# Performance work log

Hardware: AMD Instinct MI355X
Metric: run time of the kernel (lower is better)

The kernel has to match this reference:

```python
import jax, jax.numpy as jnp
import numpy as np

N = 100000      # nodes
E = 1600000     # edges (before self-loops)
IN = 256        # in_channels
HID = 16        # num_hid (per-head channels, layer 1)
HEADS = 4
OUT = 16        # out_channels (per-head channels, layer 2)
NEG_SLOPE = 0.2 # PyG GATConv default


def setup_inputs() -> dict:
    key = jax.random.key(0)
    ks = jax.random.split(key, 12)
    def glorot(k, shape, fan):
        return jax.random.normal(k, shape, jnp.float32) * (1.0 / np.sqrt(fan))
    x = jax.random.normal(ks[0], (N, IN), jnp.float32)
    edge_index = jax.random.randint(ks[1], (2, E), 0, N, dtype=jnp.int32)
    W1 = glorot(ks[2], (IN, HEADS * HID), IN)
    att_src1 = glorot(ks[3], (HEADS, HID), HID)
    att_dst1 = glorot(ks[4], (HEADS, HID), HID)
    b1 = jnp.zeros((HEADS * HID,), jnp.float32)
    W2 = glorot(ks[5], (HEADS * HID, HEADS * OUT), HEADS * HID)
    att_src2 = glorot(ks[6], (HEADS, OUT), OUT)
    att_dst2 = glorot(ks[7], (HEADS, OUT), OUT)
    b2 = jnp.zeros((HEADS * OUT,), jnp.float32)
    return {"x": x, "edge_index": edge_index, "W1": W1, "att_src1": att_src1,
            "att_dst1": att_dst1, "b1": b1, "W2": W2, "att_src2": att_src2,
            "att_dst2": att_dst2, "b2": b2}


def gat_conv(x, W, att_src, att_dst, bias, src, dst):
    # PyG GATConv (concat=True): h = xW per head; alpha via segment-softmax over dst.
    H, C = att_src.shape
    n = x.shape[0]
    h = (x @ W).reshape(n, H, C)                    # [N,H,C]
    a_s = jnp.sum(h * att_src, axis=-1)             # [N,H]
    a_d = jnp.sum(h * att_dst, axis=-1)             # [N,H]
    e = jax.nn.leaky_relu(a_s[src] + a_d[dst], NEG_SLOPE)  # [E',H]
    m = jax.lax.stop_gradient(jax.ops.segment_max(e, dst, num_segments=n))
    p = jnp.exp(e - m[dst])
    s = jax.ops.segment_sum(p, dst, num_segments=n)
    alpha = p / (s[dst] + 1e-16)                    # [E',H]
    msg = h[src] * alpha[:, :, None]                # [E',H,C] gathered messages
    out = jax.ops.segment_sum(msg, dst, num_segments=n)
    return out.reshape(n, H * C) + bias


def reference(x, edge_index, W1, att_src1, att_dst1, b1, W2, att_src2, att_dst2, b2):
    # add self loops (PyG GATConv default add_self_loops=True)
    loops = jnp.arange(N, dtype=edge_index.dtype)
    src = jnp.concatenate([edge_index[0], loops])
    dst = jnp.concatenate([edge_index[1], loops])
    h = jax.nn.relu(gat_conv(x, W1, att_src1, att_dst1, b1, src, dst))
    # dropout is identity in eval mode
    return gat_conv(h, W2, att_src2, att_dst2, b2, src, dst)
```

## Files before the change

### kernel.cpp

```cpp
#include <hip/hip_runtime.h>
#include <hip/hip_fp16.h>
#include <cstdint>


#define CH 4096
#define MAXB 512
#define SCAP 6144

using f16x8 = __attribute__((ext_vector_type(8))) _Float16;
using f32x4 = __attribute__((ext_vector_type(4))) float;

__device__ __forceinline__ float lrelu(float v) { return fmaxf(v, 0.2f * v); }

__global__ void ifill_kernel(int* __restrict__ p, int v, int n) {
  int i = blockIdx.x * blockDim.x + threadIdx.x;
  if (i < n) p[i] = v;
}

__global__ void wprep2_kernel(const float* __restrict__ W,
                              const float* __restrict__ as,
                              const float* __restrict__ ad,
                              ushort* __restrict__ WT, int K) {
  int i = blockIdx.x * 256 + threadIdx.x;
  if (i >= 80 * K) return;
  int c = i / K, k = i % K;
  float v = 0.f;
  if (c < 64) {
    v = W[k * 64 + c];
  } else if (c < 68) {
    int hd = c - 64;
    for (int j = 0; j < 16; ++j) v += W[k * 64 + hd * 16 + j] * as[hd * 16 + j];
  } else if (c < 72) {
    int hd = c - 68;
    for (int j = 0; j < 16; ++j) v += W[k * 64 + hd * 16 + j] * ad[hd * 16 + j];
  }
  WT[c * K + k] = __half_as_ushort(__float2half_rn(v));
}

__global__ __launch_bounds__(256) void bucket_hist(const int* __restrict__ edst,
                                                   int E, int nbuck,
                                                   int* __restrict__ bucket_cnt) {
  __shared__ int hist[MAXB];
  const int t = threadIdx.x;
  for (int j = t; j < MAXB; j += 256) hist[j] = 0;
  __syncthreads();
  const int base = blockIdx.x * CH;
#pragma unroll
  for (int k = 0; k < CH / 256; ++k) {
    int e = base + k * 256 + t;
    if (e < E) atomicAdd(&hist[edst[e] >> 8], 1);
  }
  __syncthreads();
  for (int j = t; j < nbuck; j += 256) {
    int c = hist[j];
    if (c) atomicAdd(&bucket_cnt[j], c);
  }
}

__global__ __launch_bounds__(512) void bucket_scan(const int* __restrict__ bucket_cnt,
                                                   int* __restrict__ bucket_base,
                                                   int* __restrict__ bucket_cursor,
                                                   int nbuck) {
  __shared__ int part[512];
  const int t = threadIdx.x;
  int v = (t < nbuck) ? bucket_cnt[t] : 0;
  part[t] = v;
  __syncthreads();
  for (int off = 1; off < 512; off <<= 1) {
    int u = (t >= off) ? part[t - off] : 0;
    __syncthreads();
    part[t] += u;
    __syncthreads();
  }
  int ex = part[t] - v;
  if (t <= nbuck) {
    int w = (t < nbuck) ? ex : part[nbuck - 1];
    bucket_base[t] = w;
    if (t < nbuck) bucket_cursor[t] = w;
  }
}

__global__ __launch_bounds__(256) void place_kernel(const int* __restrict__ esrc,
                                                    const int* __restrict__ edst,
                                                    int E, int nbuck,
                                                    int* __restrict__ bucket_cursor,
                                                    unsigned int* __restrict__ pairs) {
  __shared__ int hist[MAXB];
  __shared__ int gbase[MAXB];
  __shared__ int rcnt[MAXB];
  const int t = threadIdx.x;
  for (int j = t; j < MAXB; j += 256) { hist[j] = 0; rcnt[j] = 0; }
  __syncthreads();
  const int base = blockIdx.x * CH;
  int b_[CH / 256];
  unsigned int p_[CH / 256];
#pragma unroll
  for (int k = 0; k < CH / 256; ++k) {
    int e = base + k * 256 + t;
    if (e < E) {
      int d = edst[e];
      int s = esrc[e];
      b_[k] = d >> 8;
      p_[k] = ((unsigned int)s << 8) | (unsigned int)(d & 255);
      atomicAdd(&hist[b_[k]], 1);
    } else {
      b_[k] = -1;
    }
  }
  __syncthreads();
  for (int j = t; j < nbuck; j += 256) {
    int c = hist[j];
    gbase[j] = c ? atomicAdd(&bucket_cursor[j], c) : 0;
  }
  __syncthreads();
#pragma unroll
  for (int k = 0; k < CH / 256; ++k) {
    if (b_[k] >= 0) {
      int r = atomicAdd(&rcnt[b_[k]], 1);
      pairs[gbase[b_[k]] + r] = p_[k];
    }
  }
}

__global__ __launch_bounds__(256) void bucket_build(
    const unsigned int* __restrict__ pairs, const int* __restrict__ bucket_base,
    int* __restrict__ ccol, int* __restrict__ start, int* __restrict__ endp,
    int n) {
  __shared__ int cnt[256];
  __shared__ int ls[256];
  __shared__ int csave[256];
  __shared__ int part[256];
  __shared__ int sorted[SCAP];
  const int t = threadIdx.x;
  const int b = blockIdx.x;
  const int d0 = b << 8;
  const int DR = min(256, n - d0);
  const int in_base = bucket_base[b];
  const int nloc = bucket_base[b + 1] - in_base;
  const int out_base = in_base + d0;

  cnt[t] = (t < DR) ? 1 : 0;
  __syncthreads();
  for (int i = t; i < nloc; i += 256)
    atomicAdd(&cnt[pairs[in_base + i] & 255u], 1);
  __syncthreads();
  int c = cnt[t];
  csave[t] = c;
  part[t] = c;
  __syncthreads();
#pragma unroll
  for (int off = 1; off < 256; off <<= 1) {
    int u = (t >= off) ? part[t - off] : 0;
    __syncthreads();
    part[t] += u;
    __syncthreads();
  }
  ls[t] = part[t] - c;
  __syncthreads();
  if (t < DR) {
    int s = out_base + ls[t];
    start[d0 + t] = s;
    endp[d0 + t] = s + csave[t];
    sorted[ls[t]] = d0 + t;
    cnt[t] = 1;
  }
  __syncthreads();
  for (int i = t; i < nloc; i += 256) {
    unsigned int p = pairs[in_base + i];
    int j = (int)(p & 255u);
    int r = atomicAdd(&cnt[j], 1);
    int pos = ls[j] + r;
    if (pos < SCAP) sorted[pos] = (int)(p >> 8);
  }
  __syncthreads();
  int tot = nloc + DR;
  if (tot > SCAP) tot = SCAP;
  for (int i = t; i < tot; i += 256) ccol[out_base + i] = sorted[i];
}

__global__ __launch_bounds__(256) void gemm1_mfma(
    const float* __restrict__ x, const ushort* __restrict__ wt,
    __half* __restrict__ h, float* __restrict__ as_, float* __restrict__ ad_,
    int n) {
  constexpr int K = 256, NS = K / 32;
  __shared__ _Float16 hs[64 * 88];
  __shared__ float att[64 * 12];
  const int tid = threadIdx.x;
  const int w = tid >> 6;
  const int lane = tid & 63;
  const int lr = lane & 15;
  const int kg = lane >> 4;
  const int row0 = blockIdx.x * 64;

  int rr = row0 + w * 16 + lr;
  if (rr > n - 1) rr = n - 1;

  const ushort* wbase = wt + lr * K + kg * 8;

  f16x8 af[NS];
  {
    float4 av[NS][2];
    const float* xp = x + (long long)rr * K + kg * 8;
#pragma unroll
    for (int s = 0; s < NS; ++s) {
      av[s][0] = *(const float4*)(xp + s * 32);
      av[s][1] = *(const float4*)(xp + s * 32 + 4);
    }
#pragma unroll
    for (int s = 0; s < NS; ++s) {
      af[s][0] = (_Float16)av[s][0].x; af[s][1] = (_Float16)av[s][0].y;
      af[s][2] = (_Float16)av[s][0].z; af[s][3] = (_Float16)av[s][0].w;
      af[s][4] = (_Float16)av[s][1].x; af[s][5] = (_Float16)av[s][1].y;
      af[s][6] = (_Float16)av[s][1].z; af[s][7] = (_Float16)av[s][1].w;
    }
  }

  f32x4 acc[5] = {};
#pragma unroll
  for (int s = 0; s < NS; ++s)
#pragma unroll
    for (int ct = 0; ct < 5; ++ct) {
      f16x8 b = *(const f16x8*)(wbase + ct * 16 * K + s * 32);
      acc[ct] = __builtin_amdgcn_mfma_f32_16x16x32_f16(af[s], b, acc[ct], 0, 0, 0);
    }

  const int orow = w * 16 + kg * 4;
#pragma unroll
  for (int ct = 0; ct < 4; ++ct)
#pragma unroll
    for (int r = 0; r < 4; ++r)
      hs[(orow + r) * 88 + ct * 16 + lr] = (_Float16)acc[ct][r];
  if (lr < 8) {
#pragma unroll
    for (int r = 0; r < 4; ++r)
      att[(orow + r) * 12 + lr] = acc[4][r];
  }
  __syncthreads();
#pragma unroll
  for (int j = 0; j < 2; ++j) {
    int s = tid + j * 256;
    int row = s >> 3, seg = s & 7;
    if (row0 + row < n)
      *(uint4*)(h + (long long)(row0 + row) * 64 + seg * 8) =
          *(const uint4*)&hs[row * 88 + seg * 8];
  }
  if (tid < 64) {
    if (row0 + tid < n)
      *(float4*)(as_ + (long long)(row0 + tid) * 4) = *(const float4*)&att[tid * 12];
  } else if (tid < 128) {
    int t2 = tid - 64;
    if (row0 + t2 < n)
      *(float4*)(ad_ + (long long)(row0 + t2) * 4) = *(const float4*)&att[t2 * 12 + 4];
  }
}

__global__ __launch_bounds__(256) void agg1_kernel(
    const int* __restrict__ ccol, const int* __restrict__ start,
    const int* __restrict__ endp,
    const float* __restrict__ as1, const float* __restrict__ ad1,
    const __half2* __restrict__ h2in, const float* __restrict__ bias,
    const float* __restrict__ W2, const float* __restrict__ a2s,
    const float* __restrict__ a2d,
    __half2* __restrict__ h2out, float* __restrict__ as2,
    float* __restrict__ ad2, int n) {
  __shared__ float x2s[8][65];
  __shared__ __half2 w2s[64 * 32];
  const int t = threadIdx.x;
  for (int i = t; i < 2048; i += 256) {
    float2 wv = *(const float2*)(W2 + i * 2);
    w2s[i] = __floats2half2_rn(wv.x, wv.y);
  }

  const int lw = t >> 5;
  const int hl = t & 31;
  const int hh = hl >> 3;
  const int node = blockIdx.x * 8 + lw;
  const bool act = node < n;
  const int nodec = act ? node : 0;

  const float adv = ad1[nodec * 4 + hh];
  const int s0i = start[nodec];
  const int d = act ? (endp[nodec] - s0i) : 0;
  const int* cp = ccol + s0i;
  float ax = 0.f, ay = 0.f, den = 0.f;
  int i = 0;
  for (; i + 4 <= d; i += 4) {
    int s0 = cp[i], s1 = cp[i + 1], s2 = cp[i + 2], s3 = cp[i + 3];
    float p0 = __expf(lrelu(as1[s0 * 4 + hh] + adv));
    float p1 = __expf(lrelu(as1[s1 * 4 + hh] + adv));
    float p2 = __expf(lrelu(as1[s2 * 4 + hh] + adv));
    float p3 = __expf(lrelu(as1[s3 * 4 + hh] + adv));
    float2 h0 = __half22float2(h2in[s0 * 32 + hl]);
    float2 h1 = __half22float2(h2in[s1 * 32 + hl]);
    float2 h2v = __half22float2(h2in[s2 * 32 + hl]);
    float2 h3 = __half22float2(h2in[s3 * 32 + hl]);
    den += (p0 + p1) + (p2 + p3);
    ax = fmaf(p0, h0.x, ax); ay = fmaf(p0, h0.y, ay);
    ax = fmaf(p1, h1.x, ax); ay = fmaf(p1, h1.y, ay);
    ax = fmaf(p2, h2v.x, ax); ay = fmaf(p2, h2v.y, ay);
    ax = fmaf(p3, h3.x, ax); ay = fmaf(p3, h3.y, ay);
  }
  for (; i < d; ++i) {
    int s0 = cp[i];
    float p0 = __expf(lrelu(as1[s0 * 4 + hh] + adv));
    float2 h0 = __half22float2(h2in[s0 * 32 + hl]);
    den += p0;
    ax = fmaf(p0, h0.x, ax); ay = fmaf(p0, h0.y, ay);
  }
  const float inv = 1.0f / (den + 1e-16f);
  float vx = act ? fmaxf(ax * inv + bias[hl * 2], 0.f) : 0.f;
  float vy = act ? fmaxf(ay * inv + bias[hl * 2 + 1], 0.f) : 0.f;
  x2s[lw][hl * 2] = vx;
  x2s[lw][hl * 2 + 1] = vy;
  __syncthreads();

  float a0 = 0.f, a1 = 0.f;
#pragma unroll 8
  for (int k = 0; k < 64; ++k) {
    float xk = x2s[lw][k];
    float2 wv = __half22float2(w2s[k * 32 + hl]);
    a0 = fmaf(xk, wv.x, a0);
    a1 = fmaf(xk, wv.y, a1);
  }
  if (act) h2out[node * 32 + hl] = __floats2half2_rn(a0, a1);

  const int j0 = (hl * 2) & 15;
  float ps = a0 * a2s[hh * 16 + j0] + a1 * a2s[hh * 16 + j0 + 1];
  float pd = a0 * a2d[hh * 16 + j0] + a1 * a2d[hh * 16 + j0 + 1];
  ps += __shfl_xor(ps, 1); ps += __shfl_xor(ps, 2); ps += __shfl_xor(ps, 4);
  pd += __shfl_xor(pd, 1); pd += __shfl_xor(pd, 2); pd += __shfl_xor(pd, 4);
  if ((hl & 7) == 0 && act) {
    as2[node * 4 + hh] = ps;
    ad2[node * 4 + hh] = pd;
  }
}

__global__ __launch_bounds__(256) void agg2_kernel(
    const int* __restrict__ ccol, const int* __restrict__ start,
    const int* __restrict__ endp,
    const float* __restrict__ as2, const float* __restrict__ ad2,
    const __half2* __restrict__ h2, const float* __restrict__ bias,
    float* __restrict__ out, int n) {
  const int node = blockIdx.x * 8 + (threadIdx.x >> 5);
  if (node >= n) return;
  const int hl = threadIdx.x & 31;
  const int hh = hl >> 3;
  const float adv = ad2[node * 4 + hh];
  const int s0i = start[node];
  const int d = endp[node] - s0i;
  const int* cp = ccol + s0i;
  float ax = 0.f, ay = 0.f, den = 0.f;
  int i = 0;
  for (; i + 4 <= d; i += 4) {
    int s0 = cp[i], s1 = cp[i + 1], s2 = cp[i + 2], s3 = cp[i + 3];
    float p0 = __expf(lrelu(as2[s0 * 4 + hh] + adv));
    float p1 = __expf(lrelu(as2[s1 * 4 + hh] + adv));
    float p2 = __expf(lrelu(as2[s2 * 4 + hh] + adv));
    float p3 = __expf(lrelu(as2[s3 * 4 + hh] + adv));
    float2 h0 = __half22float2(h2[s0 * 32 + hl]);
    float2 h1 = __half22float2(h2[s1 * 32 + hl]);
    float2 h2v = __half22float2(h2[s2 * 32 + hl]);
    float2 h3 = __half22float2(h2[s3 * 32 + hl]);
    den += (p0 + p1) + (p2 + p3);
    ax = fmaf(p0, h0.x, ax); ay = fmaf(p0, h0.y, ay);
    ax = fmaf(p1, h1.x, ax); ay = fmaf(p1, h1.y, ay);
    ax = fmaf(p2, h2v.x, ax); ay = fmaf(p2, h2v.y, ay);
    ax = fmaf(p3, h3.x, ax); ay = fmaf(p3, h3.y, ay);
  }
  for (; i < d; ++i) {
    int s0 = cp[i];
    float p0 = __expf(lrelu(as2[s0 * 4 + hh] + adv));
    float2 h0 = __half22float2(h2[s0 * 32 + hl]);
    den += p0;
    ax = fmaf(p0, h0.x, ax); ay = fmaf(p0, h0.y, ay);
  }
  const float inv = 1.0f / (den + 1e-16f);
  float vx = ax * inv + bias[hl * 2];
  float vy = ay * inv + bias[hl * 2 + 1];
  *(float2*)(out + (long long)node * 64 + hl * 2) = make_float2(vx, vy);
}

extern "C" void kernel_launch(void* const* d_in, const int* in_sizes, int n_in,
                              void* d_out, int out_size, void* d_ws, size_t ws_size,
                              hipStream_t stream) {
  const float* x = (const float*)d_in[0];
  const int* ei = (const int*)d_in[1];
  const float* W1 = (const float*)d_in[2];
  const float* att_s1 = (const float*)d_in[3];
  const float* att_d1 = (const float*)d_in[4];
  const float* b1 = (const float*)d_in[5];
  const float* W2 = (const float*)d_in[6];
  const float* att_s2 = (const float*)d_in[7];
  const float* att_d2 = (const float*)d_in[8];
  const float* b2 = (const float*)d_in[9];

  const int n = in_sizes[0] / 256;
  const int E = in_sizes[1] / 2;
  const int* esrc = ei;
  const int* edst = ei + E;
  const int nbuck = (n + 255) >> 8;

  float* wsf = (float*)d_ws;
  __half* hbuf = (__half*)wsf;
  __half* h2buf = (__half*)(wsf + (long long)n * 32);
  float* as1 = wsf + (long long)n * 64;
  float* ad1 = as1 + (long long)n * 4;
  float* as2 = ad1 + (long long)n * 4;
  float* ad2 = as2 + (long long)n * 4;
  int* bucket_cnt = (int*)(ad2 + (long long)n * 4);
  int* bucket_base = bucket_cnt + MAXB;
  int* bucket_cursor = bucket_base + MAXB + 1;
  int* start = bucket_cursor + MAXB;
  int* endp = start + n;
  unsigned int* pairs = (unsigned int*)(endp + n);
  int* ccol = (int*)(pairs + E);
  ushort* wt1 = (ushort*)(((uintptr_t)(ccol + E + n) + 15) & ~(uintptr_t)15);
  float* out = (float*)d_out;

  const int ebk = (E + CH - 1) / CH;
  const int gb = (n + 63) / 64;
  const int nb1 = (n + 7) / 8;

  wprep2_kernel<<<(80 * 256 + 255) / 256, 256, 0, stream>>>(W1, att_s1, att_d1, wt1, 256);

  ifill_kernel<<<(MAXB + 255) / 256, 256, 0, stream>>>(bucket_cnt, 0, MAXB);
  bucket_hist<<<ebk, 256, 0, stream>>>(edst, E, nbuck, bucket_cnt);
  bucket_scan<<<1, 512, 0, stream>>>(bucket_cnt, bucket_base, bucket_cursor, nbuck);
  place_kernel<<<ebk, 256, 0, stream>>>(esrc, edst, E, nbuck, bucket_cursor, pairs);
  bucket_build<<<nbuck, 256, 0, stream>>>(pairs, bucket_base, ccol, start, endp, n);

  gemm1_mfma<<<gb, 256, 0, stream>>>(x, wt1, hbuf, as1, ad1, n);
  agg1_kernel<<<nb1, 256, 0, stream>>>(ccol, start, endp, as1, ad1,
                                       (const __half2*)hbuf, b1,
                                       W2, att_s2, att_d2,
                                       (__half2*)h2buf, as2, ad2, n);

  agg2_kernel<<<nb1, 256, 0, stream>>>(ccol, start, endp, as2, ad2,
                                       (const __half2*)h2buf, b2, out, n);
}
```

Measured before the change: 236.0 us.

## Compute layer-2 projection in agg1 with MFMA and prepped fp16 weights

The fused layer-2 linear projection inside agg1 switches from a scalar FMA loop over shared-memory fp32/half2 weights to MFMA 16x16x32 f16 instructions. The weights, with the attention vectors folded in as extra columns, are prepared once by a second wprep2 launch. Blocks grow to 320 threads handling 10 nodes, padded to 16 MFMA rows. Outputs are staged in shared memory for vectorised stores, and the attention logits come directly from the MFMA result. This removes per-block weight conversion and the shuffle reductions, at the cost of wasted padded rows, fp16 rounding of activations, and an extra small kernel launch.

```diff
diff --git a/kernel.cpp b/kernel.cpp
--- a/kernel.cpp
+++ b/kernel.cpp
@@ -254,27 +254,26 @@
   }
 }
 
-__global__ __launch_bounds__(256) void agg1_kernel(
+__global__ __launch_bounds__(320) void agg1_kernel(
     const int* __restrict__ ccol, const int* __restrict__ start,
     const int* __restrict__ endp,
     const float* __restrict__ as1, const float* __restrict__ ad1,
     const __half2* __restrict__ h2in, const float* __restrict__ bias,
-    const float* __restrict__ W2, const float* __restrict__ a2s,
-    const float* __restrict__ a2d,
-    __half2* __restrict__ h2out, float* __restrict__ as2,
+    const ushort* __restrict__ wt2,
+    __half* __restrict__ h2out, float* __restrict__ as2,
     float* __restrict__ ad2, int n) {
-  __shared__ float x2s[8][65];
-  __shared__ __half2 w2s[64 * 32];
+  __shared__ _Float16 x2s[16 * 72];
+  __shared__ _Float16 hs2[16 * 72];
+  __shared__ float att2[16 * 12];
   const int t = threadIdx.x;
-  for (int i = t; i < 2048; i += 256) {
-    float2 wv = *(const float2*)(W2 + i * 2);
-    w2s[i] = __floats2half2_rn(wv.x, wv.y);
-  }
+
+  for (int i = t; i < 6 * 72; i += 320) x2s[10 * 72 + i] = (_Float16)0.f;
+  if (t < 80) x2s[(t >> 3) * 72 + 64 + (t & 7)] = (_Float16)0.f;
 
   const int lw = t >> 5;
   const int hl = t & 31;
   const int hh = hl >> 3;
-  const int node = blockIdx.x * 8 + lw;
+  const int node = blockIdx.x * 10 + lw;
   const bool act = node < n;
   const int nodec = act ? node : 0;
 
@@ -310,28 +309,49 @@
   const float inv = 1.0f / (den + 1e-16f);
   float vx = act ? fmaxf(ax * inv + bias[hl * 2], 0.f) : 0.f;
   float vy = act ? fmaxf(ay * inv + bias[hl * 2 + 1], 0.f) : 0.f;
-  x2s[lw][hl * 2] = vx;
-  x2s[lw][hl * 2 + 1] = vy;
-  __syncthreads();
-
-  float a0 = 0.f, a1 = 0.f;
-#pragma unroll 8
-  for (int k = 0; k < 64; ++k) {
-    float xk = x2s[lw][k];
-    float2 wv = __half22float2(w2s[k * 32 + hl]);
-    a0 = fmaf(xk, wv.x, a0);
-    a1 = fmaf(xk, wv.y, a1);
-  }
-  if (act) h2out[node * 32 + hl] = __floats2half2_rn(a0, a1);
-
-  const int j0 = (hl * 2) & 15;
-  float ps = a0 * a2s[hh * 16 + j0] + a1 * a2s[hh * 16 + j0 + 1];
-  float pd = a0 * a2d[hh * 16 + j0] + a1 * a2d[hh * 16 + j0 + 1];
-  ps += __shfl_xor(ps, 1); ps += __shfl_xor(ps, 2); ps += __shfl_xor(ps, 4);
-  pd += __shfl_xor(pd, 1); pd += __shfl_xor(pd, 2); pd += __shfl_xor(pd, 4);
-  if ((hl & 7) == 0 && act) {
-    as2[node * 4 + hh] = ps;
-    ad2[node * 4 + hh] = pd;
+  x2s[lw * 72 + hl * 2] = (_Float16)vx;
+  x2s[lw * 72 + hl * 2 + 1] = (_Float16)vy;
+  __syncthreads();
+
+  {
+    const int w = t >> 6;
+    const int lane = t & 63;
+    const int lr = lane & 15;
+    const int kg = lane >> 4;
+    const ushort* wb = wt2 + (w * 16 + lr) * 64 + kg * 8;
+    f32x4 acc = {};
+#pragma unroll
+    for (int s = 0; s < 2; ++s) {
+      f16x8 a = *(const f16x8*)&x2s[lr * 72 + s * 32 + kg * 8];
+      f16x8 b = *(const f16x8*)(wb + s * 32);
+      acc = __builtin_amdgcn_mfma_f32_16x16x32_f16(a, b, acc, 0, 0, 0);
+    }
+    if (w < 4) {
+#pragma unroll
+      for (int r = 0; r < 4; ++r)
+        hs2[(kg * 4 + r) * 72 + w * 16 + lr] = (_Float16)acc[r];
+    } else if (lr < 8) {
+#pragma unroll
+      for (int r = 0; r < 4; ++r)
+        att2[(kg * 4 + r) * 12 + lr] = acc[r];
+    }
+  }
+  __syncthreads();
+
+  if (t < 80) {
+    int row = t >> 3, seg = t & 7;
+    int gn = blockIdx.x * 10 + row;
+    if (gn < n)
+      *(uint4*)(h2out + (long long)gn * 64 + seg * 8) =
+          *(const uint4*)&hs2[row * 72 + seg * 8];
+  } else if (t < 90) {
+    int row = t - 80;
+    int gn = blockIdx.x * 10 + row;
+    if (gn < n) *(float4*)(as2 + (long long)gn * 4) = *(const float4*)&att2[row * 12];
+  } else if (t < 100) {
+    int row = t - 90;
+    int gn = blockIdx.x * 10 + row;
+    if (gn < n) *(float4*)(ad2 + (long long)gn * 4) = *(const float4*)&att2[row * 12 + 4];
   }
 }
 
@@ -415,13 +435,16 @@
   unsigned int* pairs = (unsigned int*)(endp + n);
   int* ccol = (int*)(pairs + E);
   ushort* wt1 = (ushort*)(((uintptr_t)(ccol + E + n) + 15) & ~(uintptr_t)15);
+  ushort* wt2 = wt1 + 80 * 256;
   float* out = (float*)d_out;
 
   const int ebk = (E + CH - 1) / CH;
   const int gb = (n + 63) / 64;
-  const int nb1 = (n + 7) / 8;
+  const int nb1 = (n + 9) / 10;
+  const int nb2 = (n + 7) / 8;
 
   wprep2_kernel<<<(80 * 256 + 255) / 256, 256, 0, stream>>>(W1, att_s1, att_d1, wt1, 256);
+  wprep2_kernel<<<(80 * 64 + 255) / 256, 256, 0, stream>>>(W2, att_s2, att_d2, wt2, 64);
 
   ifill_kernel<<<(MAXB + 255) / 256, 256, 0, stream>>>(bucket_cnt, 0, MAXB);
   bucket_hist<<<ebk, 256, 0, stream>>>(edst, E, nbuck, bucket_cnt);
@@ -430,11 +453,10 @@
   bucket_build<<<nbuck, 256, 0, stream>>>(pairs, bucket_base, ccol, start, endp, n);
 
   gemm1_mfma<<<gb, 256, 0, stream>>>(x, wt1, hbuf, as1, ad1, n);
-  agg1_kernel<<<nb1, 256, 0, stream>>>(ccol, start, endp, as1, ad1,
-                                       (const __half2*)hbuf, b1,
-                                       W2, att_s2, att_d2,
-                                       (__half2*)h2buf, as2, ad2, n);
-
-  agg2_kernel<<<nb1, 256, 0, stream>>>(ccol, start, endp, as2, ad2,
+  agg1_kernel<<<nb1, 320, 0, stream>>>(ccol, start, endp, as1, ad1,
+                                       (const __half2*)hbuf, b1, wt2,
+                                       h2buf, as2, ad2, n);
+
+  agg2_kernel<<<nb2, 256, 0, stream>>>(ccol, start, endp, as2, ad2,
                                        (const __half2*)h2buf, b2, out, n);
 }
```

Result: no change. 234.3 us (-0.7%).
